# Kernel optimization log

Measured on AMD Instinct MI355X. Metric: run time of the kernel, lower is better.

Reference implementation:

```python
import jax, jax.numpy as jnp
import numpy as np

T, B, H, SEQ = 64, 512, 512, 384


def setup_inputs() -> dict:
    key = jax.random.key(0)
    k1, k2 = jax.random.split(key)
    inputs = jax.random.normal(k1, (T, B, H), dtype=jnp.float32)
    initial_hidden = jax.random.uniform(k2, (H,), dtype=jnp.float32)
    # ops in {-1, 0, 1}; rewrite pops that would underflow pos below 0 to holds
    # (the original module has no protection, so valid usage keeps pos >= 0).
    rng = np.random.default_rng(0)
    ops_raw = rng.integers(-1, 2, size=(T, B))
    pos = np.zeros(B, dtype=np.int64)
    ops = np.empty((T, B), dtype=np.int32)
    for t in range(T):
        op = ops_raw[t]
        op = np.where(pos + op < 0, 0, op)
        pos = pos + op
        ops[t] = op
    return {
        "inputs": inputs,
        "initial_hidden": initial_hidden,
        "ops": jnp.asarray(ops),
        "seq_len": SEQ,
    }


def reference(inputs, initial_hidden, ops, seq_len):
    # inputs: (T, B, H) float; ops: (T, B) int32 in {-1,0,1}
    T_, B_, H_ = inputs.shape
    bidx = jnp.arange(B_)
    # build_stack: (seq_len+2, B, H), row 0 = initial_hidden broadcast, pos = 0
    stack0 = jnp.zeros((seq_len + 2, B_, H_), dtype=inputs.dtype)
    stack0 = stack0.at[0].set(jnp.broadcast_to(initial_hidden, (B_, H_)))
    pos0 = jnp.zeros((B_,), dtype=jnp.int32)

    def step(carry, xs):
        stack, pos = carry
        x, op = xs
        # scatter-write input at pos+1 per batch element
        stack = stack.at[pos + 1, bidx].set(x)
        # pos update
        pos = pos + op
        # gather-read at updated pos
        hidden = stack[pos, bidx]  # (B, H)
        return (stack, pos), hidden

    (_, _), hiddens = jax.lax.scan(step, (stack0, pos0), (inputs, ops))
    return hiddens  # (T, B, H)
```

## Files before the change

### kernel.cpp

```cpp
#include <hip/hip_runtime.h>

#define T_DIM 64
#define B_DIM 512
#define H_DIM 512
#define H4    (H_DIM / 4)

__global__ void compute_src_kernel(const int* __restrict__ ops,
                                   int* __restrict__ src) {
    int b = blockIdx.x * blockDim.x + threadIdx.x;
    if (b >= B_DIM) return;
    int writers[T_DIM + 2];
#pragma unroll
    for (int i = 0; i < T_DIM + 2; ++i) writers[i] = -1;
    int pos = 0;
    for (int t = 0; t < T_DIM; ++t) {
        writers[pos + 1] = t;
        pos += ops[t * B_DIM + b];
        src[t * B_DIM + b] = writers[pos];
    }
}

__global__ __launch_bounds__(256) void gather_kernel(
        const float4* __restrict__ in, const float4* __restrict__ init,
        const int* __restrict__ src, float4* __restrict__ out) {
    int idx = blockIdx.x * blockDim.x + threadIdx.x;
    int row = idx >> 7;
    int h4  = idx & (H4 - 1);
    int s   = src[row];
    int b   = row & (B_DIM - 1);
    const float4* p = (s < 0)
        ? (init + h4)
        : (in + ((size_t)(s * B_DIM + b)) * H4 + h4);
    out[idx] = *p;
}

extern "C" void kernel_launch(void* const* d_in, const int* in_sizes, int n_in,
                              void* d_out, int out_size, void* d_ws, size_t ws_size,
                              hipStream_t stream) {
    const float* inputs = (const float*)d_in[0];
    const float* init   = (const float*)d_in[1];
    const int*   ops    = (const int*)d_in[2];

    int* src = (int*)d_ws;

    compute_src_kernel<<<(B_DIM + 255) / 256, 256, 0, stream>>>(ops, src);

    const int total4 = T_DIM * B_DIM * H4;
    gather_kernel<<<total4 / 256, 256, 0, stream>>>(
        (const float4*)inputs, (const float4*)init, src, (float4*)d_out);
}
```

Measured before the change: 136.8 us.

## Fuse source-index computation into gather via wave prefix scan and bitmask lookup

Replaces the serial per-batch source-index kernel and the separate gather kernel with one kernel. Each wave recomputes stack positions for its batch column with a shuffle-based prefix sum, then finds the latest writer of each position with shared-memory bitmask atomics and a count-leading-zeros. It then copies rows using nontemporal stores. This removes the second launch, the workspace round trip and the serial 64-step loop, at the cost of redoing the scan in every wave and relying on wave-level barriers.

```diff
diff --git a/kernel.cpp b/kernel.cpp
--- a/kernel.cpp
+++ b/kernel.cpp
@@ -5,33 +5,51 @@
 #define H_DIM 512
 #define H4    (H_DIM / 4)
 
-__global__ void compute_src_kernel(const int* __restrict__ ops,
-                                   int* __restrict__ src) {
-    int b = blockIdx.x * blockDim.x + threadIdx.x;
-    if (b >= B_DIM) return;
-    int writers[T_DIM + 2];
+typedef float vfloat4 __attribute__((ext_vector_type(4)));
+
+__global__ __launch_bounds__(256) void state_stack_fused(
+        const vfloat4* __restrict__ in,
+        const vfloat4* __restrict__ init,
+        const int*     __restrict__ ops,
+        vfloat4*       __restrict__ out) {
+    const int b    = blockIdx.x >> 2;
+    const int tq   = blockIdx.x & 3;
+    const int wave = threadIdx.x >> 6;
+    const int lane = threadIdx.x & 63;
+
+    const int op = ops[lane * B_DIM + b];
+    int pos = op;
 #pragma unroll
-    for (int i = 0; i < T_DIM + 2; ++i) writers[i] = -1;
-    int pos = 0;
-    for (int t = 0; t < T_DIM; ++t) {
-        writers[pos + 1] = t;
-        pos += ops[t * B_DIM + b];
-        src[t * B_DIM + b] = writers[pos];
+    for (int d = 1; d < 64; d <<= 1) {
+        int n = __shfl_up(pos, d, 64);
+        if (lane >= d) pos += n;
     }
-}
+    const int w = pos - op + 1;
 
-__global__ __launch_bounds__(256) void gather_kernel(
-        const float4* __restrict__ in, const float4* __restrict__ init,
-        const int* __restrict__ src, float4* __restrict__ out) {
-    int idx = blockIdx.x * blockDim.x + threadIdx.x;
-    int row = idx >> 7;
-    int h4  = idx & (H4 - 1);
-    int s   = src[row];
-    int b   = row & (B_DIM - 1);
-    const float4* p = (s < 0)
-        ? (init + h4)
-        : (in + ((size_t)(s * B_DIM + b)) * H4 + h4);
-    out[idx] = *p;
+    __shared__ unsigned long long masks[4][65];
+    masks[wave][lane] = 0ull;
+    if (lane == 0) masks[wave][64] = 0ull;
+    __builtin_amdgcn_wave_barrier();
+    atomicOr(&masks[wave][w], 1ull << lane);
+    __builtin_amdgcn_wave_barrier();
+    unsigned long long m = masks[wave][pos];
+    m &= (lane == 63) ? ~0ull : ((1ull << (lane + 1)) - 1ull);
+    const int my_src = m ? (63 - __builtin_clzll(m)) : -1;
+
+    const int t0 = tq * 16 + wave * 4;
+#pragma unroll
+    for (int r = 0; r < 4; ++r) {
+        const int t = t0 + r;
+        const int s = __shfl(my_src, t, 64);
+        const vfloat4* src_row = (s < 0)
+            ? init
+            : in + ((size_t)(s * B_DIM + b)) * H4;
+        const vfloat4 v0 = src_row[lane];
+        const vfloat4 v1 = src_row[lane + 64];
+        vfloat4* dst = out + ((size_t)(t * B_DIM + b)) * H4;
+        __builtin_nontemporal_store(v0, dst + lane);
+        __builtin_nontemporal_store(v1, dst + lane + 64);
+    }
 }
 
 extern "C" void kernel_launch(void* const* d_in, const int* in_sizes, int n_in,
@@ -41,11 +59,6 @@
     const float* init   = (const float*)d_in[1];
     const int*   ops    = (const int*)d_in[2];
 
-    int* src = (int*)d_ws;
-
-    compute_src_kernel<<<(B_DIM + 255) / 256, 256, 0, stream>>>(ops, src);
-
-    const int total4 = T_DIM * B_DIM * H4;
-    gather_kernel<<<total4 / 256, 256, 0, stream>>>(
-        (const float4*)inputs, (const float4*)init, src, (float4*)d_out);
+    state_stack_fused<<<B_DIM * 4, 256, 0, stream>>>(
+        (const vfloat4*)inputs, (const vfloat4*)init, ops, (vfloat4*)d_out);
 }
```

New measurement: 120.7 us. -11.8%, faster.
